# Optimization experiments

Measured on AMD Instinct MI355X. Metric: run time of the kernel, lower is better.

## Reference

```python
import jax, jax.numpy as jnp
import numpy as np

jax.config.update("jax_enable_x64", True)

P = 2038074743          # prime used by the ROBE-Z hash
BLOCK_K = 32            # tile sizes of the hashed reconstruction (kernel tile)
BLOCK_N = 32
INPUT_DIM = 8192
OUTPUT_DIM = 8192
HASH_SIZE = 1 << 22     # compressed parameter count
TOKENS = 512


def setup_inputs() -> dict:
    key = jax.random.key(0)
    k1, k2 = jax.random.split(key, 2)
    x = jax.random.normal(k1, (TOKENS, INPUT_DIM), dtype=jnp.float32)
    hashed_weight = jax.random.normal(k2, (HASH_SIZE,), dtype=jnp.float32) * 0.02
    bias = jnp.zeros((OUTPUT_DIM,), dtype=jnp.float32)
    # mirrors RzLinear._generate_random_numbers(seed): 4 random ints made even, prepended with P
    rng = np.random.RandomState(1024)
    r = rng.randint(0, P, size=(4,)).astype(np.int64)
    r = r + (r % 2)
    random_numbers = jnp.asarray(np.concatenate([np.array([P], dtype=np.int64), r]), dtype=jnp.int64)
    return {"x": x, "hashed_weight": hashed_weight, "bias": bias, "random_numbers": random_numbers}


def _weight_indices(random_numbers):
    """Hashed flat indices into hashed_weight for the dense [K, N] weight."""
    K, N = INPUT_DIM, OUTPUT_DIM
    kt, nt = K // BLOCK_K, N // BLOCK_N
    R1, R2, R3 = random_numbers[1], random_numbers[2], random_numbers[3]
    k_ids = jnp.arange(kt, dtype=jnp.int64)
    n_ids = jnp.arange(nt, dtype=jnp.int64)
    # per-tile start offset into the compressed array
    start = ((k_ids[:, None] * R3 + n_ids[None, :] * R2 + R1) % P) % (HASH_SIZE - BLOCK_K * BLOCK_N + 1)
    start = start.astype(jnp.int32)  # [kt, nt]
    off = (jnp.arange(BLOCK_K, dtype=jnp.int32)[:, None] * BLOCK_N
           + jnp.arange(BLOCK_N, dtype=jnp.int32)[None, :])  # [BK, BN], row-major within tile
    idx = start[:, None, :, None] + off[None, :, None, :]    # [kt, BK, nt, BN]
    return idx.reshape(K, N)


def reference(x, hashed_weight, bias, random_numbers):
    idx = _weight_indices(random_numbers)          # [K, N] int32
    W = hashed_weight[idx]                          # hashed-gather reconstruction, [K, N]
    out = jnp.matmul(x, W) + bias[None, :]          # [tokens, N]
    return out
```

## Files before the change

### kernel.cpp

```cpp
#include <hip/hip_runtime.h>
#include <hip/hip_fp16.h>

#define NDIM 8192
#define KDIM 8192
#define NT 256
#define MOD2 4193281
#define PRIME 2038074743LL

#define BM 256
#define BN 128
#define BK 32
#define KITER 64
#define BSLAB 1032

typedef _Float16 half8 __attribute__((ext_vector_type(8)));
typedef float floatx4 __attribute__((ext_vector_type(4)));

__global__ __launch_bounds__(256) void prep_kernel(const float* __restrict__ x,
                                                   const float* __restrict__ hw,
                                                   const float* __restrict__ bias,
                                                   const int* __restrict__ rn,
                                                   __half* __restrict__ xh,
                                                   __half* __restrict__ hh,
                                                   int* __restrict__ starts,
                                                   float* __restrict__ out) {
    int b = blockIdx.x;
    int tid = threadIdx.x;
    if (b < 8192) {
        int i = b * 256 + tid;
        const float4* s; __half2* d; int j;
        if (i < (1 << 20)) { s = (const float4*)x;  d = (__half2*)xh; j = i; }
        else               { s = (const float4*)hw; d = (__half2*)hh; j = i - (1 << 20); }
        float4 v = s[j];
        d[j * 2]     = __floats2half2_rn(v.x, v.y);
        d[j * 2 + 1] = __floats2half2_rn(v.z, v.w);
    } else if (b < 8192 + 4096) {
        int i = (b - 8192) * 256 + tid;
        float4 bv = *(const float4*)(bias + ((i & 2047) << 2));
        ((float4*)out)[i] = bv;
    } else {
        int t = (b - 12288) * 256 + tid;
        bool is64 = (rn[1] == 0 && rn[3] == 0);
        long long R1 = is64 ? rn[2] : rn[1];
        long long R2 = is64 ? rn[4] : rn[2];
        long long R3 = is64 ? rn[6] : rn[3];
        long long k_id = t >> 8, n_id = t & 255;
        long long v = (k_id * R3 + n_id * R2 + R1) % PRIME;
        starts[t] = (int)(v % MOD2);
    }
}

__device__ __forceinline__ void gload16(const __half* g, __half* l) {
    __builtin_amdgcn_global_load_lds((const __attribute__((address_space(1))) void*)g,
                                     (__attribute__((address_space(3))) void*)l, 16, 0, 0);
}

#define SBAR() __builtin_amdgcn_sched_barrier(0)

__global__ __launch_bounds__(512, 4) void gemm_kernel(
    const __half* __restrict__ xh, const __half* __restrict__ hh,
    const int* __restrict__ starts, float* __restrict__ out) {
    __shared__ __align__(16) __half As[2][BM * 32];
    __shared__ __align__(16) __half Bs[2][4 * BSLAB];
    __shared__ int Ss[KITER * 4];

    const int tid = threadIdx.x;
    const int lane = tid & 63;
    const int wave = tid >> 6;
    const int wm = wave >> 1;
    const int wn = wave & 1;
    const int quad = lane >> 4;
    const int l16 = lane & 15;

    const int i = blockIdx.x;
    const int ks = i & 3;
    const int m_blk = (i >> 2) & 1;
    const int n_blk = i >> 3;
    const int gm0 = m_blk * BM;
    const int gn0 = n_blk * BN;
    const int kt0 = ks * KITER;
    const int n_id0 = n_blk * 4;

    if (tid < KITER * 4) {
        int kp = tid >> 2, tile = tid & 3;
        Ss[tid] = starts[(kt0 + kp) * NT + n_id0 + tile];
    }

    const int a_t = wave * 2;
    const int a_chunk = (lane & 3) ^ ((lane >> 3) & 3);
    const __half* a_g0 = xh + (size_t)(gm0 + a_t * 16 + (lane >> 2)) * KDIM
                         + kt0 * 32 + a_chunk * 8;
    const __half* a_g1 = a_g0 + (size_t)16 * KDIM;

#define STAGE_A(buf_, kp_) do {                                                \
        gload16(a_g0 + (kp_) * 32, &As[buf_][a_t * 512]);                      \
        gload16(a_g1 + (kp_) * 32, &As[buf_][a_t * 512 + 512]);                \
    } while (0)

    const int b_tile = tid >> 7;
    const int t7 = tid & 127;
    const int b_np = t7 & 15;
    const int b_kg = t7 >> 4;
    const int b_oct = b_kg >> 1;
    const unsigned b_base = b_oct * BSLAB;
    const unsigned b_pos = (b_tile * 32 + 2 * b_np) * 8 + (b_kg & 1) * 4;
    const unsigned bswz = (b_np & 4) << 1;

    unsigned pbA0, pbA1, pbA2, pbA3, pbB0, pbB1, pbB2, pbB3;

#define LOADT(Q0, Q1, Q2, Q3, kp_) do {                                        \
        int st = Ss[(kp_) * 4 + b_tile];                                       \
        const __half* src = hh + st + b_kg * 128 + b_np * 2;                   \
        Q0 = *(const unsigned*)(src);                                          \
        Q1 = *(const unsigned*)(src + 32);                                     \
        Q2 = *(const unsigned*)(src + 64);                                     \
        Q3 = *(const unsigned*)(src + 96);                                     \
    } while (0)

#define STORET(Q0, Q1, Q2, Q3, buf_) do {                                      \
        unsigned lo0 = (Q0 & 0xffffu) | (Q1 << 16);                            \
        unsigned lo1 = (Q2 & 0xffffu) | (Q3 << 16);                            \
        unsigned hi0 = (Q0 >> 16) | (Q1 & 0xffff0000u);                        \
        unsigned hi1 = (Q2 >> 16) | (Q3 & 0xffff0000u);                        \
        uint2 e = {lo0, lo1}, o = {hi0, hi1};                                  \
        *(uint2*)&Bs[buf_][b_base + (b_pos ^ bswz)] = e;                       \
        *(uint2*)&Bs[buf_][b_base + ((b_pos + 8) ^ bswz)] = o;                 \
    } while (0)

    floatx4 acc[4][4];
#pragma unroll
    for (int r = 0; r < 4; r++)
#pragma unroll
        for (int c = 0; c < 4; c++)
            acc[r][c] = (floatx4){0.f, 0.f, 0.f, 0.f};

    const unsigned rswz = (unsigned)(l16 & 8);
    const unsigned a_rswz = (unsigned)((l16 >> 1) & 3);

    half8 fa0, fa1, fa2, fa3, fb0, fb1, fb2, fb3;

#define READF(buf_) do {                                                       \
        fa0 = *(const half8*)&As[buf_][(unsigned)(wm * 64 +  0 + l16) * 32 + ((quad ^ a_rswz) * 8)]; \
        fa1 = *(const half8*)&As[buf_][(unsigned)(wm * 64 + 16 + l16) * 32 + ((quad ^ a_rswz) * 8)]; \
        fa2 = *(const half8*)&As[buf_][(unsigned)(wm * 64 + 32 + l16) * 32 + ((quad ^ a_rswz) * 8)]; \
        fa3 = *(const half8*)&As[buf_][(unsigned)(wm * 64 + 48 + l16) * 32 + ((quad ^ a_rswz) * 8)]; \
        fb0 = *(const half8*)&Bs[buf_][quad * BSLAB + ((unsigned)((wn * 64 +  0 + l16) * 8) ^ rswz)]; \
        fb1 = *(const half8*)&Bs[buf_][quad * BSLAB + ((unsigned)((wn * 64 + 16 + l16) * 8) ^ rswz)]; \
        fb2 = *(const half8*)&Bs[buf_][quad * BSLAB + ((unsigned)((wn * 64 + 32 + l16) * 8) ^ rswz)]; \
        fb3 = *(const half8*)&Bs[buf_][quad * BSLAB + ((unsigned)((wn * 64 + 48 + l16) * 8) ^ rswz)]; \
    } while (0)

#define MFMAC() do {                                                           \
        __builtin_amdgcn_s_setprio(1);                                         \
        acc[0][0] = __builtin_amdgcn_mfma_f32_16x16x32_f16(fa0, fb0, acc[0][0], 0, 0, 0); \
        acc[1][0] = __builtin_amdgcn_mfma_f32_16x16x32_f16(fa1, fb0, acc[1][0], 0, 0, 0); \
        acc[2][0] = __builtin_amdgcn_mfma_f32_16x16x32_f16(fa2, fb0, acc[2][0], 0, 0, 0); \
        acc[3][0] = __builtin_amdgcn_mfma_f32_16x16x32_f16(fa3, fb0, acc[3][0], 0, 0, 0); \
        acc[0][1] = __builtin_amdgcn_mfma_f32_16x16x32_f16(fa0, fb1, acc[0][1], 0, 0, 0); \
        acc[1][1] = __builtin_amdgcn_mfma_f32_16x16x32_f16(fa1, fb1, acc[1][1], 0, 0, 0); \
        acc[2][1] = __builtin_amdgcn_mfma_f32_16x16x32_f16(fa2, fb1, acc[2][1], 0, 0, 0); \
        acc[3][1] = __builtin_amdgcn_mfma_f32_16x16x32_f16(fa3, fb1, acc[3][1], 0, 0, 0); \
        acc[0][2] = __builtin_amdgcn_mfma_f32_16x16x32_f16(fa0, fb2, acc[0][2], 0, 0, 0); \
        acc[1][2] = __builtin_amdgcn_mfma_f32_16x16x32_f16(fa1, fb2, acc[1][2], 0, 0, 0); \
        acc[2][2] = __builtin_amdgcn_mfma_f32_16x16x32_f16(fa2, fb2, acc[2][2], 0, 0, 0); \
        acc[3][2] = __builtin_amdgcn_mfma_f32_16x16x32_f16(fa3, fb2, acc[3][2], 0, 0, 0); \
        acc[0][3] = __builtin_amdgcn_mfma_f32_16x16x32_f16(fa0, fb3, acc[0][3], 0, 0, 0); \
        acc[1][3] = __builtin_amdgcn_mfma_f32_16x16x32_f16(fa1, fb3, acc[1][3], 0, 0, 0); \
        acc[2][3] = __builtin_amdgcn_mfma_f32_16x16x32_f16(fa2, fb3, acc[2][3], 0, 0, 0); \
        acc[3][3] = __builtin_amdgcn_mfma_f32_16x16x32_f16(fa3, fb3, acc[3][3], 0, 0, 0); \
        __builtin_amdgcn_s_setprio(0);                                         \
    } while (0)

    __syncthreads();
    STAGE_A(0, 0);
    LOADT(pbA0, pbA1, pbA2, pbA3, 0);
    LOADT(pbB0, pbB1, pbB2, pbB3, 1);
    STORET(pbA0, pbA1, pbA2, pbA3, 0);
    __syncthreads();

    for (int kp = 0; kp < KITER; kp += 2) {
        READF(0);
        STAGE_A(1, kp + 1);
        if (kp + 2 < KITER) LOADT(pbA0, pbA1, pbA2, pbA3, kp + 2);
        SBAR();
        __builtin_amdgcn_s_barrier();
        SBAR();
        MFMAC();
        STORET(pbB0, pbB1, pbB2, pbB3, 1);
        SBAR();
        if (kp + 2 < KITER)
            __builtin_amdgcn_s_waitcnt(0x0074);
        else
            __builtin_amdgcn_s_waitcnt(0x0070);
        __builtin_amdgcn_s_barrier();
        SBAR();

        READF(1);
        if (kp + 2 < KITER) STAGE_A(0, kp + 2);
        if (kp + 3 < KITER) LOADT(pbB0, pbB1, pbB2, pbB3, kp + 3);
        SBAR();
        __builtin_amdgcn_s_barrier();
        SBAR();
        MFMAC();
        if (kp + 2 < KITER)
            STORET(pbA0, pbA1, pbA2, pbA3, 0);
        SBAR();
        __builtin_amdgcn_s_waitcnt(0x0074);
        __builtin_amdgcn_s_barrier();
        SBAR();
    }

#pragma unroll
    for (int c = 0; c < 4; c++) {
        int col = gn0 + wn * 64 + c * 16 + l16;
#pragma unroll
        for (int r = 0; r < 4; r++) {
            int row0 = gm0 + wm * 64 + r * 16 + quad * 4;
#pragma unroll
            for (int e = 0; e < 4; e++)
                atomicAdd(&out[(size_t)(row0 + e) * NDIM + col], acc[r][c][e]);
        }
    }
#undef LOADT
#undef STORET
#undef READF
#undef MFMAC
#undef STAGE_A
}

extern "C" void kernel_launch(void* const* d_in, const int* in_sizes, int n_in,
                              void* d_out, int out_size, void* d_ws, size_t ws_size,
                              hipStream_t stream) {
    const float* x = (const float*)d_in[0];
    const float* hw = (const float*)d_in[1];
    const float* bias = (const float*)d_in[2];
    const int* rn = (const int*)d_in[3];
    float* out = (float*)d_out;

    char* ws = (char*)d_ws;
    __half* xh = (__half*)ws;
    __half* hh = (__half*)(ws + (8u << 20));
    int* starts = (int*)(ws + (16u << 20));

    hipLaunchKernelGGL(prep_kernel, dim3(12544), dim3(256), 0, stream,
                       x, hw, bias, rn, xh, hh, starts, out);
    hipLaunchKernelGGL(gemm_kernel, dim3(512), dim3(512), 0, stream, xh, hh, starts, out);
}
```

Baseline: 192.2 us.

## Triple-buffer LDS tiles with rotating indices to prefetch A two steps ahead

Grows the A and B LDS tiles from two buffers to three and rotates buffer indices every half-iteration. The A tile is now staged two k-steps ahead, so global-to-LDS load latency gets more time to overlap with MFMA work. The explicit barrier wait now only drains LDS operations, relying on the compiler's register-dependency waits and in-order vmcnt completion to cover the A loads. The larger LDS footprint can lower how many blocks fit per CU, and the relaxed wait adds a correctness risk if those ordering assumptions fail.

```diff
diff --git a/kernel.cpp b/kernel.cpp
--- a/kernel.cpp
+++ b/kernel.cpp
@@ -56,12 +56,13 @@
 }
 
 #define SBAR() __builtin_amdgcn_sched_barrier(0)
+#define WAIT_LGKM0() __builtin_amdgcn_s_waitcnt(0xC07F)
 
 __global__ __launch_bounds__(512, 4) void gemm_kernel(
     const __half* __restrict__ xh, const __half* __restrict__ hh,
     const int* __restrict__ starts, float* __restrict__ out) {
-    __shared__ __align__(16) __half As[2][BM * 32];
-    __shared__ __align__(16) __half Bs[2][4 * BSLAB];
+    __shared__ __align__(16) __half As[3][BM * 32];
+    __shared__ __align__(16) __half Bs[3][4 * BSLAB];
     __shared__ int Ss[KITER * 4];
 
     const int tid = threadIdx.x;
@@ -92,9 +93,9 @@
                          + kt0 * 32 + a_chunk * 8;
     const __half* a_g1 = a_g0 + (size_t)16 * KDIM;
 
-#define STAGE_A(buf_, kp_) do {                                                \
-        gload16(a_g0 + (kp_) * 32, &As[buf_][a_t * 512]);                      \
-        gload16(a_g1 + (kp_) * 32, &As[buf_][a_t * 512 + 512]);                \
+#define STAGE_A(c_, kp_) do {                                                  \
+        gload16(a_g0 + (kp_) * 32, &As[c_][a_t * 512]);                        \
+        gload16(a_g1 + (kp_) * 32, &As[c_][a_t * 512 + 512]);                  \
     } while (0)
 
     const int b_tile = tid >> 7;
@@ -117,14 +118,14 @@
         Q3 = *(const unsigned*)(src + 96);                                     \
     } while (0)
 
-#define STORET(Q0, Q1, Q2, Q3, buf_) do {                                      \
+#define STORET(Q0, Q1, Q2, Q3, c_) do {                                        \
         unsigned lo0 = (Q0 & 0xffffu) | (Q1 << 16);                            \
         unsigned lo1 = (Q2 & 0xffffu) | (Q3 << 16);                            \
         unsigned hi0 = (Q0 >> 16) | (Q1 & 0xffff0000u);                        \
         unsigned hi1 = (Q2 >> 16) | (Q3 & 0xffff0000u);                        \
         uint2 e = {lo0, lo1}, o = {hi0, hi1};                                  \
-        *(uint2*)&Bs[buf_][b_base + (b_pos ^ bswz)] = e;                       \
-        *(uint2*)&Bs[buf_][b_base + ((b_pos + 8) ^ bswz)] = o;                 \
+        *(uint2*)&Bs[c_][b_base + (b_pos ^ bswz)] = e;                         \
+        *(uint2*)&Bs[c_][b_base + ((b_pos + 8) ^ bswz)] = o;                   \
     } while (0)
 
     floatx4 acc[4][4];
@@ -139,15 +140,15 @@
 
     half8 fa0, fa1, fa2, fa3, fb0, fb1, fb2, fb3;
 
-#define READF(buf_) do {                                                       \
-        fa0 = *(const half8*)&As[buf_][(unsigned)(wm * 64 +  0 + l16) * 32 + ((quad ^ a_rswz) * 8)]; \
-        fa1 = *(const half8*)&As[buf_][(unsigned)(wm * 64 + 16 + l16) * 32 + ((quad ^ a_rswz) * 8)]; \
-        fa2 = *(const half8*)&As[buf_][(unsigned)(wm * 64 + 32 + l16) * 32 + ((quad ^ a_rswz) * 8)]; \
-        fa3 = *(const half8*)&As[buf_][(unsigned)(wm * 64 + 48 + l16) * 32 + ((quad ^ a_rswz) * 8)]; \
-        fb0 = *(const half8*)&Bs[buf_][quad * BSLAB + ((unsigned)((wn * 64 +  0 + l16) * 8) ^ rswz)]; \
-        fb1 = *(const half8*)&Bs[buf_][quad * BSLAB + ((unsigned)((wn * 64 + 16 + l16) * 8) ^ rswz)]; \
-        fb2 = *(const half8*)&Bs[buf_][quad * BSLAB + ((unsigned)((wn * 64 + 32 + l16) * 8) ^ rswz)]; \
-        fb3 = *(const half8*)&Bs[buf_][quad * BSLAB + ((unsigned)((wn * 64 + 48 + l16) * 8) ^ rswz)]; \
+#define READF(c_) do {                                                         \
+        fa0 = *(const half8*)&As[c_][(unsigned)(wm * 64 +  0 + l16) * 32 + ((quad ^ a_rswz) * 8)]; \
+        fa1 = *(const half8*)&As[c_][(unsigned)(wm * 64 + 16 + l16) * 32 + ((quad ^ a_rswz) * 8)]; \
+        fa2 = *(const half8*)&As[c_][(unsigned)(wm * 64 + 32 + l16) * 32 + ((quad ^ a_rswz) * 8)]; \
+        fa3 = *(const half8*)&As[c_][(unsigned)(wm * 64 + 48 + l16) * 32 + ((quad ^ a_rswz) * 8)]; \
+        fb0 = *(const half8*)&Bs[c_][quad * BSLAB + ((unsigned)((wn * 64 +  0 + l16) * 8) ^ rswz)]; \
+        fb1 = *(const half8*)&Bs[c_][quad * BSLAB + ((unsigned)((wn * 64 + 16 + l16) * 8) ^ rswz)]; \
+        fb2 = *(const half8*)&Bs[c_][quad * BSLAB + ((unsigned)((wn * 64 + 32 + l16) * 8) ^ rswz)]; \
+        fb3 = *(const half8*)&Bs[c_][quad * BSLAB + ((unsigned)((wn * 64 + 48 + l16) * 8) ^ rswz)]; \
     } while (0)
 
 #define MFMAC() do {                                                           \
@@ -171,43 +172,54 @@
         __builtin_amdgcn_s_setprio(0);                                         \
     } while (0)
 
+    unsigned ca = 0, cb = 1, cc = 2, ct;
+#define ROT() do { ct = ca; ca = cb; cb = cc; cc = ct; } while (0)
+
     __syncthreads();
     STAGE_A(0, 0);
+    SBAR();
     LOADT(pbA0, pbA1, pbA2, pbA3, 0);
+    STAGE_A(1, 1);
+    SBAR();
     LOADT(pbB0, pbB1, pbB2, pbB3, 1);
     STORET(pbA0, pbA1, pbA2, pbA3, 0);
     __syncthreads();
 
     for (int kp = 0; kp < KITER; kp += 2) {
-        READF(0);
-        STAGE_A(1, kp + 1);
-        if (kp + 2 < KITER) LOADT(pbA0, pbA1, pbA2, pbA3, kp + 2);
+        READF(ca);
+        if (kp + 2 < KITER) {
+            STAGE_A(cc, kp + 2);
+            SBAR();
+            LOADT(pbA0, pbA1, pbA2, pbA3, kp + 2);
+        }
         SBAR();
         __builtin_amdgcn_s_barrier();
         SBAR();
         MFMAC();
-        STORET(pbB0, pbB1, pbB2, pbB3, 1);
-        SBAR();
-        if (kp + 2 < KITER)
-            __builtin_amdgcn_s_waitcnt(0x0074);
-        else
-            __builtin_amdgcn_s_waitcnt(0x0070);
-        __builtin_amdgcn_s_barrier();
-        SBAR();
-
-        READF(1);
-        if (kp + 2 < KITER) STAGE_A(0, kp + 2);
-        if (kp + 3 < KITER) LOADT(pbB0, pbB1, pbB2, pbB3, kp + 3);
+        STORET(pbB0, pbB1, pbB2, pbB3, cb);
+        SBAR();
+        WAIT_LGKM0();
+        __builtin_amdgcn_s_barrier();
+        SBAR();
+        ROT();
+
+        READF(ca);
+        if (kp + 3 < KITER) {
+            STAGE_A(cc, kp + 3);
+            SBAR();
+            LOADT(pbB0, pbB1, pbB2, pbB3, kp + 3);
+        }
         SBAR();
         __builtin_amdgcn_s_barrier();
         SBAR();
         MFMAC();
         if (kp + 2 < KITER)
-            STORET(pbA0, pbA1, pbA2, pbA3, 0);
-        SBAR();
-        __builtin_amdgcn_s_waitcnt(0x0074);
-        __builtin_amdgcn_s_barrier();
-        SBAR();
+            STORET(pbA0, pbA1, pbA2, pbA3, cb);
+        SBAR();
+        WAIT_LGKM0();
+        __builtin_amdgcn_s_barrier();
+        SBAR();
+        ROT();
     }
 
 #pragma unroll
@@ -226,6 +238,7 @@
 #undef READF
 #undef MFMAC
 #undef STAGE_A
+#undef ROT
 }
 
 extern "C" void kernel_launch(void* const* d_in, const int* in_sizes, int n_in,
```

Result: no change. 195.7 us (+1.8%).

## Halve GEMM block to 256 threads with 128x64 warp tiles

Applied to the files above, without the earlier changes.

Drops the GEMM workgroup from 512 to 256 threads and doubles each wave's M-extent, so each wave computes a 128x64 output sub-tile (32 accumulators, 8 A fragments) and loads twice as much A and B per thread. This gives more MFMA work per LDS fragment read and fewer barrier participants. In exchange it roughly doubles accumulator and prefetch register use, which can lower occupancy or cause spills. The waitcnt values are adjusted for the larger number of outstanding loads.

```diff
diff --git a/kernel.cpp b/kernel.cpp
--- a/kernel.cpp
+++ b/kernel.cpp
@@ -57,7 +57,7 @@
 
 #define SBAR() __builtin_amdgcn_sched_barrier(0)
 
-__global__ __launch_bounds__(512, 4) void gemm_kernel(
+__global__ __launch_bounds__(256, 2) void gemm_kernel(
     const __half* __restrict__ xh, const __half* __restrict__ hh,
     const int* __restrict__ starts, float* __restrict__ out) {
     __shared__ __align__(16) __half As[2][BM * 32];
@@ -81,55 +81,71 @@
     const int kt0 = ks * KITER;
     const int n_id0 = n_blk * 4;
 
-    if (tid < KITER * 4) {
+    {
         int kp = tid >> 2, tile = tid & 3;
         Ss[tid] = starts[(kt0 + kp) * NT + n_id0 + tile];
     }
 
-    const int a_t = wave * 2;
+    const int a_w4 = wave * 4;
     const int a_chunk = (lane & 3) ^ ((lane >> 3) & 3);
-    const __half* a_g0 = xh + (size_t)(gm0 + a_t * 16 + (lane >> 2)) * KDIM
+    const __half* a_g0 = xh + (size_t)(gm0 + a_w4 * 16 + (lane >> 2)) * KDIM
                          + kt0 * 32 + a_chunk * 8;
     const __half* a_g1 = a_g0 + (size_t)16 * KDIM;
-
-#define STAGE_A(buf_, kp_) do {                                                \
-        gload16(a_g0 + (kp_) * 32, &As[buf_][a_t * 512]);                      \
-        gload16(a_g1 + (kp_) * 32, &As[buf_][a_t * 512 + 512]);                \
-    } while (0)
-
-    const int b_tile = tid >> 7;
-    const int t7 = tid & 127;
-    const int b_np = t7 & 15;
-    const int b_kg = t7 >> 4;
+    const __half* a_g2 = a_g0 + (size_t)32 * KDIM;
+    const __half* a_g3 = a_g0 + (size_t)48 * KDIM;
+
+#define STAGE_A(c_, kp_) do {                                                  \
+        gload16(a_g0 + (kp_) * 32, &As[c_][a_w4 * 512]);                       \
+        gload16(a_g1 + (kp_) * 32, &As[c_][a_w4 * 512 + 512]);                 \
+        gload16(a_g2 + (kp_) * 32, &As[c_][a_w4 * 512 + 1024]);                \
+        gload16(a_g3 + (kp_) * 32, &As[c_][a_w4 * 512 + 1536]);                \
+    } while (0)
+
+    const int b_tile = tid >> 6;
+    const int t6 = tid & 63;
+    const int b_np = t6 & 15;
+    const int b_kg = t6 >> 4;
     const int b_oct = b_kg >> 1;
     const unsigned b_base = b_oct * BSLAB;
     const unsigned b_pos = (b_tile * 32 + 2 * b_np) * 8 + (b_kg & 1) * 4;
     const unsigned bswz = (b_np & 4) << 1;
 
-    unsigned pbA0, pbA1, pbA2, pbA3, pbB0, pbB1, pbB2, pbB3;
-
-#define LOADT(Q0, Q1, Q2, Q3, kp_) do {                                        \
+    unsigned pbA0, pbA1, pbA2, pbA3, pbA4, pbA5, pbA6, pbA7;
+    unsigned pbB0, pbB1, pbB2, pbB3, pbB4, pbB5, pbB6, pbB7;
+
+#define LOADT(Q0, Q1, Q2, Q3, Q4, Q5, Q6, Q7, kp_) do {                        \
         int st = Ss[(kp_) * 4 + b_tile];                                       \
         const __half* src = hh + st + b_kg * 128 + b_np * 2;                   \
         Q0 = *(const unsigned*)(src);                                          \
         Q1 = *(const unsigned*)(src + 32);                                     \
         Q2 = *(const unsigned*)(src + 64);                                     \
         Q3 = *(const unsigned*)(src + 96);                                     \
-    } while (0)
-
-#define STORET(Q0, Q1, Q2, Q3, buf_) do {                                      \
+        Q4 = *(const unsigned*)(src + 512);                                    \
+        Q5 = *(const unsigned*)(src + 544);                                    \
+        Q6 = *(const unsigned*)(src + 576);                                    \
+        Q7 = *(const unsigned*)(src + 608);                                    \
+    } while (0)
+
+#define STORET(Q0, Q1, Q2, Q3, Q4, Q5, Q6, Q7, c_) do {                        \
         unsigned lo0 = (Q0 & 0xffffu) | (Q1 << 16);                            \
         unsigned lo1 = (Q2 & 0xffffu) | (Q3 << 16);                            \
         unsigned hi0 = (Q0 >> 16) | (Q1 & 0xffff0000u);                        \
         unsigned hi1 = (Q2 >> 16) | (Q3 & 0xffff0000u);                        \
-        uint2 e = {lo0, lo1}, o = {hi0, hi1};                                  \
-        *(uint2*)&Bs[buf_][b_base + (b_pos ^ bswz)] = e;                       \
-        *(uint2*)&Bs[buf_][b_base + ((b_pos + 8) ^ bswz)] = o;                 \
-    } while (0)
-
-    floatx4 acc[4][4];
-#pragma unroll
-    for (int r = 0; r < 4; r++)
+        uint2 e0 = {lo0, lo1}, o0 = {hi0, hi1};                                \
+        *(uint2*)&Bs[c_][b_base + (b_pos ^ bswz)] = e0;                        \
+        *(uint2*)&Bs[c_][b_base + ((b_pos + 8) ^ bswz)] = o0;                  \
+        unsigned lo2 = (Q4 & 0xffffu) | (Q5 << 16);                            \
+        unsigned lo3 = (Q6 & 0xffffu) | (Q7 << 16);                            \
+        unsigned hi2 = (Q4 >> 16) | (Q5 & 0xffff0000u);                        \
+        unsigned hi3 = (Q6 >> 16) | (Q7 & 0xffff0000u);                        \
+        uint2 e1 = {lo2, lo3}, o1 = {hi2, hi3};                                \
+        *(uint2*)&Bs[c_][b_base + 2 * BSLAB + (b_pos ^ bswz)] = e1;            \
+        *(uint2*)&Bs[c_][b_base + 2 * BSLAB + ((b_pos + 8) ^ bswz)] = o1;      \
+    } while (0)
+
+    floatx4 acc[8][4];
+#pragma unroll
+    for (int r = 0; r < 8; r++)
 #pragma unroll
         for (int c = 0; c < 4; c++)
             acc[r][c] = (floatx4){0.f, 0.f, 0.f, 0.f};
@@ -137,59 +153,61 @@
     const unsigned rswz = (unsigned)(l16 & 8);
     const unsigned a_rswz = (unsigned)((l16 >> 1) & 3);
 
-    half8 fa0, fa1, fa2, fa3, fb0, fb1, fb2, fb3;
-
-#define READF(buf_) do {                                                       \
-        fa0 = *(const half8*)&As[buf_][(unsigned)(wm * 64 +  0 + l16) * 32 + ((quad ^ a_rswz) * 8)]; \
-        fa1 = *(const half8*)&As[buf_][(unsigned)(wm * 64 + 16 + l16) * 32 + ((quad ^ a_rswz) * 8)]; \
-        fa2 = *(const half8*)&As[buf_][(unsigned)(wm * 64 + 32 + l16) * 32 + ((quad ^ a_rswz) * 8)]; \
-        fa3 = *(const half8*)&As[buf_][(unsigned)(wm * 64 + 48 + l16) * 32 + ((quad ^ a_rswz) * 8)]; \
-        fb0 = *(const half8*)&Bs[buf_][quad * BSLAB + ((unsigned)((wn * 64 +  0 + l16) * 8) ^ rswz)]; \
-        fb1 = *(const half8*)&Bs[buf_][quad * BSLAB + ((unsigned)((wn * 64 + 16 + l16) * 8) ^ rswz)]; \
-        fb2 = *(const half8*)&Bs[buf_][quad * BSLAB + ((unsigned)((wn * 64 + 32 + l16) * 8) ^ rswz)]; \
-        fb3 = *(const half8*)&Bs[buf_][quad * BSLAB + ((unsigned)((wn * 64 + 48 + l16) * 8) ^ rswz)]; \
-    } while (0)
+    half8 fa0, fa1, fa2, fa3, fa4, fa5, fa6, fa7, fb0, fb1, fb2, fb3;
+
+#define READF(c_) do {                                                         \
+        fa0 = *(const half8*)&As[c_][(unsigned)(wm * 128 +   0 + l16) * 32 + ((quad ^ a_rswz) * 8)]; \
+        fa1 = *(const half8*)&As[c_][(unsigned)(wm * 128 +  16 + l16) * 32 + ((quad ^ a_rswz) * 8)]; \
+        fa2 = *(const half8*)&As[c_][(unsigned)(wm * 128 +  32 + l16) * 32 + ((quad ^ a_rswz) * 8)]; \
+        fa3 = *(const half8*)&As[c_][(unsigned)(wm * 128 +  48 + l16) * 32 + ((quad ^ a_rswz) * 8)]; \
+        fa4 = *(const half8*)&As[c_][(unsigned)(wm * 128 +  64 + l16) * 32 + ((quad ^ a_rswz) * 8)]; \
+        fa5 = *(const half8*)&As[c_][(unsigned)(wm * 128 +  80 + l16) * 32 + ((quad ^ a_rswz) * 8)]; \
+        fa6 = *(const half8*)&As[c_][(unsigned)(wm * 128 +  96 + l16) * 32 + ((quad ^ a_rswz) * 8)]; \
+        fa7 = *(const half8*)&As[c_][(unsigned)(wm * 128 + 112 + l16) * 32 + ((quad ^ a_rswz) * 8)]; \
+        fb0 = *(const half8*)&Bs[c_][quad * BSLAB + ((unsigned)((wn * 64 +  0 + l16) * 8) ^ rswz)]; \
+        fb1 = *(const half8*)&Bs[c_][quad * BSLAB + ((unsigned)((wn * 64 + 16 + l16) * 8) ^ rswz)]; \
+        fb2 = *(const half8*)&Bs[c_][quad * BSLAB + ((unsigned)((wn * 64 + 32 + l16) * 8) ^ rswz)]; \
+        fb3 = *(const half8*)&Bs[c_][quad * BSLAB + ((unsigned)((wn * 64 + 48 + l16) * 8) ^ rswz)]; \
+    } while (0)
+
+#define MF(r_, c_, fa_, fb_) \
+        acc[r_][c_] = __builtin_amdgcn_mfma_f32_16x16x32_f16(fa_, fb_, acc[r_][c_], 0, 0, 0)
 
 #define MFMAC() do {                                                           \
         __builtin_amdgcn_s_setprio(1);                                         \
-        acc[0][0] = __builtin_amdgcn_mfma_f32_16x16x32_f16(fa0, fb0, acc[0][0], 0, 0, 0); \
-        acc[1][0] = __builtin_amdgcn_mfma_f32_16x16x32_f16(fa1, fb0, acc[1][0], 0, 0, 0); \
-        acc[2][0] = __builtin_amdgcn_mfma_f32_16x16x32_f16(fa2, fb0, acc[2][0], 0, 0, 0); \
-        acc[3][0] = __builtin_amdgcn_mfma_f32_16x16x32_f16(fa3, fb0, acc[3][0], 0, 0, 0); \
-        acc[0][1] = __builtin_amdgcn_mfma_f32_16x16x32_f16(fa0, fb1, acc[0][1], 0, 0, 0); \
-        acc[1][1] = __builtin_amdgcn_mfma_f32_16x16x32_f16(fa1, fb1, acc[1][1], 0, 0, 0); \
-        acc[2][1] = __builtin_amdgcn_mfma_f32_16x16x32_f16(fa2, fb1, acc[2][1], 0, 0, 0); \
-        acc[3][1] = __builtin_amdgcn_mfma_f32_16x16x32_f16(fa3, fb1, acc[3][1], 0, 0, 0); \
-        acc[0][2] = __builtin_amdgcn_mfma_f32_16x16x32_f16(fa0, fb2, acc[0][2], 0, 0, 0); \
-        acc[1][2] = __builtin_amdgcn_mfma_f32_16x16x32_f16(fa1, fb2, acc[1][2], 0, 0, 0); \
-        acc[2][2] = __builtin_amdgcn_mfma_f32_16x16x32_f16(fa2, fb2, acc[2][2], 0, 0, 0); \
-        acc[3][2] = __builtin_amdgcn_mfma_f32_16x16x32_f16(fa3, fb2, acc[3][2], 0, 0, 0); \
-        acc[0][3] = __builtin_amdgcn_mfma_f32_16x16x32_f16(fa0, fb3, acc[0][3], 0, 0, 0); \
-        acc[1][3] = __builtin_amdgcn_mfma_f32_16x16x32_f16(fa1, fb3, acc[1][3], 0, 0, 0); \
-        acc[2][3] = __builtin_amdgcn_mfma_f32_16x16x32_f16(fa2, fb3, acc[2][3], 0, 0, 0); \
-        acc[3][3] = __builtin_amdgcn_mfma_f32_16x16x32_f16(fa3, fb3, acc[3][3], 0, 0, 0); \
+        MF(0,0,fa0,fb0); MF(1,0,fa1,fb0); MF(2,0,fa2,fb0); MF(3,0,fa3,fb0);    \
+        MF(4,0,fa4,fb0); MF(5,0,fa5,fb0); MF(6,0,fa6,fb0); MF(7,0,fa7,fb0);    \
+        MF(0,1,fa0,fb1); MF(1,1,fa1,fb1); MF(2,1,fa2,fb1); MF(3,1,fa3,fb1);    \
+        MF(4,1,fa4,fb1); MF(5,1,fa5,fb1); MF(6,1,fa6,fb1); MF(7,1,fa7,fb1);    \
+        MF(0,2,fa0,fb2); MF(1,2,fa1,fb2); MF(2,2,fa2,fb2); MF(3,2,fa3,fb2);    \
+        MF(4,2,fa4,fb2); MF(5,2,fa5,fb2); MF(6,2,fa6,fb2); MF(7,2,fa7,fb2);    \
+        MF(0,3,fa0,fb3); MF(1,3,fa1,fb3); MF(2,3,fa2,fb3); MF(3,3,fa3,fb3);    \
+        MF(4,3,fa4,fb3); MF(5,3,fa5,fb3); MF(6,3,fa6,fb3); MF(7,3,fa7,fb3);    \
         __builtin_amdgcn_s_setprio(0);                                         \
     } while (0)
 
     __syncthreads();
     STAGE_A(0, 0);
-    LOADT(pbA0, pbA1, pbA2, pbA3, 0);
-    LOADT(pbB0, pbB1, pbB2, pbB3, 1);
-    STORET(pbA0, pbA1, pbA2, pbA3, 0);
+    SBAR();
+    LOADT(pbA0, pbA1, pbA2, pbA3, pbA4, pbA5, pbA6, pbA7, 0);
+    LOADT(pbB0, pbB1, pbB2, pbB3, pbB4, pbB5, pbB6, pbB7, 1);
+    STORET(pbA0, pbA1, pbA2, pbA3, pbA4, pbA5, pbA6, pbA7, 0);
     __syncthreads();
 
     for (int kp = 0; kp < KITER; kp += 2) {
         READF(0);
         STAGE_A(1, kp + 1);
-        if (kp + 2 < KITER) LOADT(pbA0, pbA1, pbA2, pbA3, kp + 2);
+        SBAR();
+        if (kp + 2 < KITER)
+            LOADT(pbA0, pbA1, pbA2, pbA3, pbA4, pbA5, pbA6, pbA7, kp + 2);
         SBAR();
         __builtin_amdgcn_s_barrier();
         SBAR();
         MFMAC();
-        STORET(pbB0, pbB1, pbB2, pbB3, 1);
+        STORET(pbB0, pbB1, pbB2, pbB3, pbB4, pbB5, pbB6, pbB7, 1);
         SBAR();
         if (kp + 2 < KITER)
-            __builtin_amdgcn_s_waitcnt(0x0074);
+            __builtin_amdgcn_s_waitcnt(0x0078);
         else
             __builtin_amdgcn_s_waitcnt(0x0070);
         __builtin_amdgcn_s_barrier();
@@ -197,15 +215,17 @@
 
         READF(1);
         if (kp + 2 < KITER) STAGE_A(0, kp + 2);
-        if (kp + 3 < KITER) LOADT(pbB0, pbB1, pbB2, pbB3, kp + 3);
+        SBAR();
+        if (kp + 3 < KITER)
+            LOADT(pbB0, pbB1, pbB2, pbB3, pbB4, pbB5, pbB6, pbB7, kp + 3);
         SBAR();
         __builtin_amdgcn_s_barrier();
         SBAR();
         MFMAC();
         if (kp + 2 < KITER)
-            STORET(pbA0, pbA1, pbA2, pbA3, 0);
-        SBAR();
-        __builtin_amdgcn_s_waitcnt(0x0074);
+            STORET(pbA0, pbA1, pbA2, pbA3, pbA4, pbA5, pbA6, pbA7, 0);
+        SBAR();
+        __builtin_amdgcn_s_waitcnt(0x0078);
         __builtin_amdgcn_s_barrier();
         SBAR();
     }
@@ -214,8 +234,8 @@
     for (int c = 0; c < 4; c++) {
         int col = gn0 + wn * 64 + c * 16 + l16;
 #pragma unroll
-        for (int r = 0; r < 4; r++) {
-            int row0 = gm0 + wm * 64 + r * 16 + quad * 4;
+        for (int r = 0; r < 8; r++) {
+            int row0 = gm0 + wm * 128 + r * 16 + quad * 4;
 #pragma unroll
             for (int e = 0; e < 4; e++)
                 atomicAdd(&out[(size_t)(row0 + e) * NDIM + col], acc[r][c][e]);
@@ -225,6 +245,7 @@
 #undef STORET
 #undef READF
 #undef MFMAC
+#undef MF
 #undef STAGE_A
 }
 
@@ -244,5 +265,5 @@
 
     hipLaunchKernelGGL(prep_kernel, dim3(12544), dim3(256), 0, stream,
                        x, hw, bias, rn, xh, hh, starts, out);
-    hipLaunchKernelGGL(gemm_kernel, dim3(512), dim3(512), 0, stream, xh, hh, starts, out);
-}
+    hipLaunchKernelGGL(gemm_kernel, dim3(512), dim3(256), 0, stream, xh, hh, starts, out);
+}
```

New measurement: 191.8 us. About the same (-0.2%).
